# Optimization experiments

Measured on AMD Instinct MI355X. Metric: run time of the kernel, lower is better.

## Reference

```python
import jax, jax.numpy as jnp
import numpy as np

N_NODES = 20000
N_EDGES = 320000
N_FEAT = 128
HID = 64
HEADS = 4
N_CLS = 16
NEG_SLOPE = 0.2


def setup_inputs() -> dict:
    key = jax.random.key(0)
    ks = jax.random.split(key, 12)
    x = jax.random.normal(ks[0], (N_NODES, N_FEAT), dtype=jnp.float32)
    edge_index = jax.random.randint(ks[1], (2, N_EDGES), 0, N_NODES, dtype=jnp.int64)
    # layer 1: GATConv(128 -> 64, heads=4, concat)
    s1 = 1.0 / np.sqrt(N_FEAT)
    W1 = jax.random.uniform(ks[2], (N_FEAT, HEADS * HID), jnp.float32, -s1, s1)
    a_src1 = jax.random.uniform(ks[3], (HEADS, HID), jnp.float32, -s1, s1)
    a_dst1 = jax.random.uniform(ks[4], (HEADS, HID), jnp.float32, -s1, s1)
    b1 = jnp.zeros((HEADS * HID,), jnp.float32)
    # layer 2: GATConv(256 -> 16, heads=1)
    s2 = 1.0 / np.sqrt(HEADS * HID)
    W2 = jax.random.uniform(ks[5], (HEADS * HID, N_CLS), jnp.float32, -s2, s2)
    a_src2 = jax.random.uniform(ks[6], (1, N_CLS), jnp.float32, -s2, s2)
    a_dst2 = jax.random.uniform(ks[7], (1, N_CLS), jnp.float32, -s2, s2)
    b2 = jnp.zeros((N_CLS,), jnp.float32)
    return {"x": x, "edge_index": edge_index, "W1": W1, "a_src1": a_src1,
            "a_dst1": a_dst1, "b1": b1, "W2": W2, "a_src2": a_src2,
            "a_dst2": a_dst2, "b2": b2}


def gat_conv(x, src, dst, W, a_src, a_dst, bias, n_nodes):
    # x: [N, F_in]; W: [F_in, H*C]; a_src/a_dst: [H, C]
    H, C = a_src.shape
    h = (x @ W).reshape(n_nodes, H, C)                     # [N, H, C]
    al_src = jnp.sum(h * a_src[None], axis=-1)             # [N, H]
    al_dst = jnp.sum(h * a_dst[None], axis=-1)             # [N, H]
    e = jax.nn.leaky_relu(al_src[src] + al_dst[dst], NEG_SLOPE)  # [E, H]
    # segment softmax over incoming edges of each destination node
    m = jax.ops.segment_max(e, dst, num_segments=n_nodes)  # [N, H]
    e = jnp.exp(e - m[dst])
    denom = jax.ops.segment_sum(e, dst, num_segments=n_nodes)
    alpha = e / (denom[dst] + 1e-16)                       # [E, H]
    msg = h[src] * alpha[:, :, None]                       # [E, H, C]
    out = jax.ops.segment_sum(msg, dst, num_segments=n_nodes)  # [N, H, C]
    return out.reshape(n_nodes, H * C) + bias


def reference(x, edge_index, W1, a_src1, a_dst1, b1, W2, a_src2, a_dst2, b2):
    n = x.shape[0]
    loops = jnp.arange(n, dtype=edge_index.dtype)
    src = jnp.concatenate([edge_index[0], loops])
    dst = jnp.concatenate([edge_index[1], loops])
    # eval mode: dropout is identity
    h = jax.nn.elu(gat_conv(x, src, dst, W1, a_src1, a_dst1, b1, n))
    out = gat_conv(h, src, dst, W2, a_src2, a_dst2, b2, n)
    return out
```

## Files before the change

### kernel.cpp

```cpp
#include <hip/hip_runtime.h>
#include <hip/hip_bf16.h>
#include <hip/hip_fp16.h>
#include <math.h>

#define N_NODES 20000
#define N_EDGES 320000
#define E_TOT   (N_EDGES + N_NODES)
#define N_FEAT  128
#define NEG_SLOPE 0.2f
#define MAXDEG  64
#define CURPAD  16

typedef _Float16 half8 __attribute__((ext_vector_type(8)));
typedef float f32x4 __attribute__((ext_vector_type(4)));

__global__ void k_init(int* __restrict__ cur,
                       const float* __restrict__ W1, _Float16* __restrict__ W1t){
  int tid = blockIdx.x * blockDim.x + threadIdx.x;
  if (tid < N_NODES * CURPAD) cur[tid] = 0;
  if (tid < 4096){
    int n = tid >> 4, ks = tid & 15;
    union { __half2 h2[4]; half8 h8; } u;
    float v[8];
    #pragma unroll
    for (int r = 0; r < 8; ++r) v[r] = W1[(size_t)(ks * 8 + r) * 256 + n];
    u.h2[0] = __floats2half2_rn(v[0], v[1]);
    u.h2[1] = __floats2half2_rn(v[2], v[3]);
    u.h2[2] = __floats2half2_rn(v[4], v[5]);
    u.h2[3] = __floats2half2_rn(v[6], v[7]);
    *(half8*)&W1t[(size_t)n * 128 + ks * 8] = u.h8;
  }
}

__global__ __launch_bounds__(256) void k_gemm1(
                        const float* __restrict__ x, const _Float16* __restrict__ W1t,
                        const float* __restrict__ as1, const float* __restrict__ ad1,
                        _Float16* __restrict__ h1h,
                        float* __restrict__ alS, float* __restrict__ alD,
                        const int* __restrict__ ei, int* __restrict__ cur,
                        int* __restrict__ adjS){
  __shared__ _Float16 xt[64][136];
  __shared__ _Float16 Wt[128][136];
  int t  = threadIdx.x;

  {
    int fb = blockIdx.y * 313 + blockIdx.x;
    int gtid = fb * 256 + t;
    const int GSZ = 313 * 2 * 256;
    int e0 = gtid, e1 = gtid + GSZ, e2 = gtid + 2 * GSZ;
    bool k2 = (e2 < E_TOT);
    int s0, d0, s1, d1, s2 = 0, d2 = 0;
    if (e0 < N_EDGES){ s0 = ei[e0]; d0 = ei[N_EDGES + e0]; } else { s0 = d0 = e0 - N_EDGES; }
    if (e1 < N_EDGES){ s1 = ei[e1]; d1 = ei[N_EDGES + e1]; } else { s1 = d1 = e1 - N_EDGES; }
    if (k2){
      if (e2 < N_EDGES){ s2 = ei[e2]; d2 = ei[N_EDGES + e2]; } else { s2 = d2 = e2 - N_EDGES; }
    }
    int p0 = atomicAdd(&cur[d0 * CURPAD], 1);
    int p1 = atomicAdd(&cur[d1 * CURPAD], 1);
    int p2 = k2 ? atomicAdd(&cur[d2 * CURPAD], 1) : 0;
    if (p0 < MAXDEG) adjS[d0 * MAXDEG + p0] = s0;
    if (p1 < MAXDEG) adjS[d1 * MAXDEG + p1] = s1;
    if (k2 && p2 < MAXDEG) adjS[d2 * MAXDEG + p2] = s2;
  }

  int m0 = blockIdx.x * 64;
  int by = blockIdx.y;
  int j0 = by * 128;
  #pragma unroll
  for (int ii = 0; ii < 4; ++ii){
    int f = t + ii * 256;
    int r = f >> 4, s = f & 15;
    half8 xv = (half8)(_Float16)0.f;
    if (m0 + r < N_NODES){
      float4 a = *(const float4*)&x[(size_t)(m0 + r) * 128 + s * 8];
      float4 bq = *(const float4*)&x[(size_t)(m0 + r) * 128 + s * 8 + 4];
      union { __half2 h2[4]; half8 h8; } u;
      u.h2[0] = __floats2half2_rn(a.x, a.y);
      u.h2[1] = __floats2half2_rn(a.z, a.w);
      u.h2[2] = __floats2half2_rn(bq.x, bq.y);
      u.h2[3] = __floats2half2_rn(bq.z, bq.w);
      xv = u.h8;
    }
    *(half8*)&xt[r][s * 8] = xv;
  }
  #pragma unroll
  for (int ii = 0; ii < 8; ++ii){
    int f = t + ii * 256;
    int r = f >> 4, s = f & 15;
    half8 wv = *(const half8*)&W1t[(size_t)(j0 + r) * 128 + s * 8];
    *(half8*)&Wt[r][s * 8] = wv;
  }
  __syncthreads();

  int w = t >> 6, lane = t & 63;
  int g = lane >> 4, mi = lane & 15;
  f32x4 acc[8] = {};
  #pragma unroll
  for (int kk = 0; kk < 4; ++kk){
    int ko = kk * 32 + g * 8;
    half8 b = *(const half8*)&xt[w * 16 + mi][ko];
    #pragma unroll
    for (int s = 0; s < 8; ++s){
      half8 a = *(const half8*)&Wt[s * 16 + mi][ko];
      acc[s] = __builtin_amdgcn_mfma_f32_16x16x32_f16(a, b, acc[s], 0, 0, 0);
    }
  }

  int m = m0 + w * 16 + mi;
  float sA = 0.f, dA = 0.f, sB = 0.f, dB = 0.f;
  #pragma unroll
  for (int s = 0; s < 8; ++s){
    int nb = j0 + s * 16 + g * 4;
    float4 asv = *(const float4*)&as1[nb];
    float4 adv = *(const float4*)&ad1[nb];
    float sv = acc[s][0] * asv.x + acc[s][1] * asv.y + acc[s][2] * asv.z + acc[s][3] * asv.w;
    float dv = acc[s][0] * adv.x + acc[s][1] * adv.y + acc[s][2] * adv.z + acc[s][3] * adv.w;
    if (s < 4){ sA += sv; dA += dv; } else { sB += sv; dB += dv; }
    if (m < N_NODES){
      union { __half2 h2[2]; float2 f2; } u;
      u.h2[0] = __floats2half2_rn(acc[s][0], acc[s][1]);
      u.h2[1] = __floats2half2_rn(acc[s][2], acc[s][3]);
      *(float2*)&h1h[(size_t)m * 256 + nb] = u.f2;
    }
  }
  sA += __shfl_xor(sA, 16); sA += __shfl_xor(sA, 32);
  dA += __shfl_xor(dA, 16); dA += __shfl_xor(dA, 32);
  sB += __shfl_xor(sB, 16); sB += __shfl_xor(sB, 32);
  dB += __shfl_xor(dB, 16); dB += __shfl_xor(dB, 32);
  if (g == 0 && m < N_NODES){
    int h0 = by * 2, h1 = by * 2 + 1;
    alS[(size_t)h0 * N_NODES + m] = sA; alD[(size_t)h0 * N_NODES + m] = dA;
    alS[(size_t)h1 * N_NODES + m] = sB; alD[(size_t)h1 * N_NODES + m] = dB;
  }
}

__global__ __launch_bounds__(256) void k_attn1(
                        const int* __restrict__ cur, const int* __restrict__ adjS,
                        const __half* __restrict__ h1h,
                        const float* __restrict__ alS, const float* __restrict__ alD,
                        const float* __restrict__ b1, _Float16* __restrict__ heluh){
  int b    = blockIdx.x;
  int slot = b & 7;
  int h    = slot & 3;
  int g    = (slot >> 2) * 625 + (b >> 3);
  int t    = threadIdx.x;
  int w    = t >> 6, lane = t & 63;
  int grp  = lane >> 4, l16 = lane & 15;
  int hf   = l16 >> 3, l8 = l16 & 7;
  int n    = g * 16 + w * 4 + grp;

  int cnt  = cur[n * CURPAD]; cnt = (cnt > MAXDEG) ? MAXDEG : cnt;
  int base = n * MAXDEG;
  const float* __restrict__ alSp = alS + (size_t)h * N_NODES;
  float ald = alD[(size_t)h * N_NODES + n];
  const __half* __restrict__ hb = h1h + h * 64 + l8 * 8;

  float4 Aa = make_float4(0.f,0.f,0.f,0.f), Ab = Aa;
  float den = 0.f;

  int nq = cnt >> 2;
  for (int q = hf; q < nq; q += 2){
    int4 quad = *(const int4*)&adjS[base + q * 4];
    int s0 = quad.x, s1 = quad.y, s2 = quad.z, s3 = quad.w;
    float t0 = alSp[s0] + ald;
    float t1 = alSp[s1] + ald;
    float t2 = alSp[s2] + ald;
    float t3 = alSp[s3] + ald;
    t0 = (t0 > 0.f) ? t0 : NEG_SLOPE * t0;
    t1 = (t1 > 0.f) ? t1 : NEG_SLOPE * t1;
    t2 = (t2 > 0.f) ? t2 : NEG_SLOPE * t2;
    t3 = (t3 > 0.f) ? t3 : NEG_SLOPE * t3;
    float w0 = __expf(t0), w1 = __expf(t1), w2 = __expf(t2), w3 = __expf(t3);
    float4 r0 = *(const float4*)&hb[(size_t)s0 * 256];
    float4 r1 = *(const float4*)&hb[(size_t)s1 * 256];
    float4 r2 = *(const float4*)&hb[(size_t)s2 * 256];
    float4 r3 = *(const float4*)&hb[(size_t)s3 * 256];
    const __half2* p0 = (const __half2*)&r0;
    const __half2* p1 = (const __half2*)&r1;
    const __half2* p2 = (const __half2*)&r2;
    const __half2* p3 = (const __half2*)&r3;
    {
      float2 a0 = __half22float2(p0[0]), a1 = __half22float2(p0[1]);
      float2 a2 = __half22float2(p0[2]), a3 = __half22float2(p0[3]);
      Aa.x += w0 * a0.x; Aa.y += w0 * a0.y; Aa.z += w0 * a1.x; Aa.w += w0 * a1.y;
      Ab.x += w0 * a2.x; Ab.y += w0 * a2.y; Ab.z += w0 * a3.x; Ab.w += w0 * a3.y;
    }
    {
      float2 a0 = __half22float2(p1[0]), a1 = __half22float2(p1[1]);
      float2 a2 = __half22float2(p1[2]), a3 = __half22float2(p1[3]);
      Aa.x += w1 * a0.x; Aa.y += w1 * a0.y; Aa.z += w1 * a1.x; Aa.w += w1 * a1.y;
      Ab.x += w1 * a2.x; Ab.y += w1 * a2.y; Ab.z += w1 * a3.x; Ab.w += w1 * a3.y;
    }
    {
      float2 a0 = __half22float2(p2[0]), a1 = __half22float2(p2[1]);
      float2 a2 = __half22float2(p2[2]), a3 = __half22float2(p2[3]);
      Aa.x += w2 * a0.x; Aa.y += w2 * a0.y; Aa.z += w2 * a1.x; Aa.w += w2 * a1.y;
      Ab.x += w2 * a2.x; Ab.y += w2 * a2.y; Ab.z += w2 * a3.x; Ab.w += w2 * a3.y;
    }
    {
      float2 a0 = __half22float2(p3[0]), a1 = __half22float2(p3[1]);
      float2 a2 = __half22float2(p3[2]), a3 = __half22float2(p3[3]);
      Aa.x += w3 * a0.x; Aa.y += w3 * a0.y; Aa.z += w3 * a1.x; Aa.w += w3 * a1.y;
      Ab.x += w3 * a2.x; Ab.y += w3 * a2.y; Ab.z += w3 * a3.x; Ab.w += w3 * a3.y;
    }
    den += ((w0 + w1) + (w2 + w3));
  }
  if ((nq & 1) == hf){
    for (int i = base + nq * 4; i < base + cnt; ++i){
      int s0 = adjS[i];
      float t0 = alSp[s0] + ald;
      t0 = (t0 > 0.f) ? t0 : NEG_SLOPE * t0;
      float w0 = __expf(t0);
      float4 r0 = *(const float4*)&hb[(size_t)s0 * 256];
      const __half2* p0 = (const __half2*)&r0;
      float2 a0 = __half22float2(p0[0]), a1 = __half22float2(p0[1]);
      float2 a2 = __half22float2(p0[2]), a3 = __half22float2(p0[3]);
      Aa.x += w0 * a0.x; Aa.y += w0 * a0.y; Aa.z += w0 * a1.x; Aa.w += w0 * a1.y;
      Ab.x += w0 * a2.x; Ab.y += w0 * a2.y; Ab.z += w0 * a3.x; Ab.w += w0 * a3.y;
      den += w0;
    }
  }
  Aa.x += __shfl_xor(Aa.x, 8); Aa.y += __shfl_xor(Aa.y, 8);
  Aa.z += __shfl_xor(Aa.z, 8); Aa.w += __shfl_xor(Aa.w, 8);
  Ab.x += __shfl_xor(Ab.x, 8); Ab.y += __shfl_xor(Ab.y, 8);
  Ab.z += __shfl_xor(Ab.z, 8); Ab.w += __shfl_xor(Ab.w, 8);
  den  += __shfl_xor(den, 8);

  if (hf == 0){
    float rinv = 1.f / (den + 1e-16f);
    float4 bv0 = *(const float4*)&b1[h * 64 + l8 * 8];
    float4 bv1 = *(const float4*)&b1[h * 64 + l8 * 8 + 4];
    float o0 = Aa.x * rinv + bv0.x;
    float o1 = Aa.y * rinv + bv0.y;
    float o2 = Aa.z * rinv + bv0.z;
    float o3 = Aa.w * rinv + bv0.w;
    float o4 = Ab.x * rinv + bv1.x;
    float o5 = Ab.y * rinv + bv1.y;
    float o6 = Ab.z * rinv + bv1.z;
    float o7 = Ab.w * rinv + bv1.w;
    o0 = (o0 > 0.f) ? o0 : (__expf(o0) - 1.f);
    o1 = (o1 > 0.f) ? o1 : (__expf(o1) - 1.f);
    o2 = (o2 > 0.f) ? o2 : (__expf(o2) - 1.f);
    o3 = (o3 > 0.f) ? o3 : (__expf(o3) - 1.f);
    o4 = (o4 > 0.f) ? o4 : (__expf(o4) - 1.f);
    o5 = (o5 > 0.f) ? o5 : (__expf(o5) - 1.f);
    o6 = (o6 > 0.f) ? o6 : (__expf(o6) - 1.f);
    o7 = (o7 > 0.f) ? o7 : (__expf(o7) - 1.f);
    union { __half2 h2[4]; half8 h8; } u;
    u.h2[0] = __floats2half2_rn(o0, o1);
    u.h2[1] = __floats2half2_rn(o2, o3);
    u.h2[2] = __floats2half2_rn(o4, o5);
    u.h2[3] = __floats2half2_rn(o6, o7);
    *(half8*)&heluh[(size_t)n * 256 + h * 64 + l8 * 8] = u.h8;
  }
}

__global__ __launch_bounds__(256) void k_gemm2(
                        const _Float16* __restrict__ heluh, const float* __restrict__ W2,
                        const float* __restrict__ as2, const float* __restrict__ ad2,
                        float* __restrict__ h2, float* __restrict__ alS, float* __restrict__ alD){
  __shared__ _Float16 Ht[64][264];
  __shared__ _Float16 Wt[16][264];
  int t = threadIdx.x;
  int n0 = blockIdx.x * 64;
  #pragma unroll
  for (int ii = 0; ii < 8; ++ii){
    int f = t + ii * 256;
    int r = f >> 5, s = f & 31;
    half8 v = (half8)(_Float16)0.f;
    if (n0 + r < N_NODES) v = *(const half8*)&heluh[(size_t)(n0 + r) * 256 + s * 8];
    *(half8*)&Ht[r][s * 8] = v;
  }
  {
    int k = t;
    float4 w0 = *(const float4*)&W2[k * 16 + 0];
    float4 w1 = *(const float4*)&W2[k * 16 + 4];
    float4 w2 = *(const float4*)&W2[k * 16 + 8];
    float4 w3 = *(const float4*)&W2[k * 16 + 12];
    float wv[16] = {w0.x,w0.y,w0.z,w0.w, w1.x,w1.y,w1.z,w1.w,
                    w2.x,w2.y,w2.z,w2.w, w3.x,w3.y,w3.z,w3.w};
    #pragma unroll
    for (int c = 0; c < 16; ++c) Wt[c][k] = (_Float16)wv[c];
  }
  __syncthreads();

  int w = t >> 6, lane = t & 63;
  int g = lane >> 4, mi = lane & 15;
  f32x4 acc = {};
  #pragma unroll
  for (int kk = 0; kk < 8; ++kk){
    int ko = kk * 32 + g * 8;
    half8 b = *(const half8*)&Ht[w * 16 + mi][ko];
    half8 a = *(const half8*)&Wt[mi][ko];
    acc = __builtin_amdgcn_mfma_f32_16x16x32_f16(a, b, acc, 0, 0, 0);
  }
  int n = n0 + w * 16 + mi;
  float4 asv = *(const float4*)&as2[g * 4];
  float4 adv = *(const float4*)&ad2[g * 4];
  float s_ = acc[0] * asv.x + acc[1] * asv.y + acc[2] * asv.z + acc[3] * asv.w;
  float d_ = acc[0] * adv.x + acc[1] * adv.y + acc[2] * adv.z + acc[3] * adv.w;
  s_ += __shfl_xor(s_, 16); s_ += __shfl_xor(s_, 32);
  d_ += __shfl_xor(d_, 16); d_ += __shfl_xor(d_, 32);
  if (n < N_NODES){
    float4 hv = make_float4(acc[0], acc[1], acc[2], acc[3]);
    *(float4*)&h2[(size_t)n * 16 + g * 4] = hv;
    if (g == 0){ alS[n] = s_; alD[n] = d_; }
  }
}

__global__ __launch_bounds__(256) void k_attn2(
                        const int* __restrict__ cur, const int* __restrict__ adjS,
                        const float* __restrict__ h2,
                        const float* __restrict__ alS, const float* __restrict__ alD,
                        const float* __restrict__ b2, float* __restrict__ out){
  int t    = threadIdx.x;
  int w    = t >> 6, lane = t & 63;
  int grp  = lane >> 4, l16 = lane & 15;
  int j    = l16 >> 2, c4 = l16 & 3;
  int n    = blockIdx.x * 16 + w * 4 + grp;

  int cnt  = cur[n * CURPAD]; cnt = (cnt > MAXDEG) ? MAXDEG : cnt;
  int start = n * MAXDEG, end = start + cnt;
  float ald = alD[n];
  float4 acc = make_float4(0.f,0.f,0.f,0.f);
  float den = 0.f;
  for (int i = start + j; i < end; i += 4){
    int s = adjS[i];
    float tt = alS[s] + ald;
    tt = (tt > 0.f) ? tt : NEG_SLOPE * tt;
    float wv = __expf(tt);
    float4 v = *(const float4*)&h2[(size_t)s * 16 + c4 * 4];
    acc.x += wv * v.x; acc.y += wv * v.y; acc.z += wv * v.z; acc.w += wv * v.w;
    den += wv;
  }
  #pragma unroll
  for (int off = 4; off <= 8; off <<= 1){
    acc.x += __shfl_xor(acc.x, off);
    acc.y += __shfl_xor(acc.y, off);
    acc.z += __shfl_xor(acc.z, off);
    acc.w += __shfl_xor(acc.w, off);
    den   += __shfl_xor(den, off);
  }
  if (j == 0){
    float rinv = 1.f / (den + 1e-16f);
    float4 bv = *(const float4*)&b2[c4 * 4];
    float4 o;
    o.x = acc.x * rinv + bv.x; o.y = acc.y * rinv + bv.y;
    o.z = acc.z * rinv + bv.z; o.w = acc.w * rinv + bv.w;
    *(float4*)&out[(size_t)n * 16 + c4 * 4] = o;
  }
}

extern "C" void kernel_launch(void* const* d_in, const int* in_sizes, int n_in,
                              void* d_out, int out_size, void* d_ws, size_t ws_size,
                              hipStream_t stream){
  const float* x   = (const float*)d_in[0];
  const int*   ei  = (const int*)d_in[1];
  const float* W1  = (const float*)d_in[2];
  const float* as1 = (const float*)d_in[3];
  const float* ad1 = (const float*)d_in[4];
  const float* b1  = (const float*)d_in[5];
  const float* W2  = (const float*)d_in[6];
  const float* as2 = (const float*)d_in[7];
  const float* ad2 = (const float*)d_in[8];
  const float* b2  = (const float*)d_in[9];
  float* out = (float*)d_out;

  float* fws = (float*)d_ws;
  size_t off = 0;
  __half* h1h = (__half*)(fws + off); off += (size_t)N_NODES * 128;
  _Float16* W1t = (_Float16*)(fws + off); off += 256 * 64;
  _Float16* heluh = (_Float16*)(fws + off); off += (size_t)N_NODES * 128;
  float* h2   = fws + off; off += (size_t)N_NODES * 16;
  float* alS1 = fws + off; off += N_NODES * 4;
  float* alD1 = fws + off; off += N_NODES * 4;
  float* alS2 = fws + off; off += N_NODES;
  float* alD2 = fws + off; off += N_NODES;
  int* cur  = (int*)(fws + off); off += (size_t)N_NODES * CURPAD;
  int* adjS = (int*)(fws + off); off += (size_t)N_NODES * MAXDEG;

  k_init<<<(N_NODES * CURPAD + 255) / 256, 256, 0, stream>>>(cur, W1, W1t);
  k_gemm1<<<dim3(313, 2), 256, 0, stream>>>(x, W1t, as1, ad1, (_Float16*)h1h,
                                            alS1, alD1, ei, cur, adjS);
  k_attn1<<<5000, 256, 0, stream>>>(cur, adjS, h1h, alS1, alD1, b1, heluh);
  k_gemm2<<<313, 256, 0, stream>>>(heluh, W2, as2, ad2, h2, alS2, alD2);
  k_attn2<<<1250, 256, 0, stream>>>(cur, adjS, h2, alS2, alD2, b2, out);
}
```

Before: 73.25 us.

## Partition adjacency build per XCD with workgroup-scope atomics

Measured after the change: 89.61 us. 1.22x slower.

```diff
diff --git a/kernel.cpp b/kernel.cpp
--- a/kernel.cpp
+++ b/kernel.cpp
@@ -8,16 +8,15 @@
 #define E_TOT   (N_EDGES + N_NODES)
 #define N_FEAT  128
 #define NEG_SLOPE 0.2f
-#define MAXDEG  64
-#define CURPAD  16
+#define SEG     64
 
 typedef _Float16 half8 __attribute__((ext_vector_type(8)));
 typedef float f32x4 __attribute__((ext_vector_type(4)));
 
-__global__ void k_init(int* __restrict__ cur,
+__global__ void k_init(int* __restrict__ cur8,
                        const float* __restrict__ W1, _Float16* __restrict__ W1t){
   int tid = blockIdx.x * blockDim.x + threadIdx.x;
-  if (tid < N_NODES * CURPAD) cur[tid] = 0;
+  if (tid < 8 * N_NODES) cur8[tid] = 0;
   if (tid < 4096){
     int n = tid >> 4, ks = tid & 15;
     union { __half2 h2[4]; half8 h8; } u;
@@ -37,13 +36,18 @@
                         const float* __restrict__ as1, const float* __restrict__ ad1,
                         _Float16* __restrict__ h1h,
                         float* __restrict__ alS, float* __restrict__ alD,
-                        const int* __restrict__ ei, int* __restrict__ cur,
-                        int* __restrict__ adjS){
+                        const int* __restrict__ ei, int* __restrict__ cur8,
+                        int* __restrict__ adjS8){
   __shared__ _Float16 xt[64][136];
   __shared__ _Float16 Wt[128][136];
   int t  = threadIdx.x;
 
   {
+    int xcd;
+    asm volatile("s_getreg_b32 %0, hwreg(HW_REG_XCC_ID)" : "=s"(xcd));
+    xcd &= 7;
+    int* __restrict__ curp = cur8 + xcd * N_NODES;
+    int* __restrict__ adjp = adjS8 + (size_t)xcd * N_NODES * SEG;
     int fb = blockIdx.y * 313 + blockIdx.x;
     int gtid = fb * 256 + t;
     const int GSZ = 313 * 2 * 256;
@@ -55,12 +59,12 @@
     if (k2){
       if (e2 < N_EDGES){ s2 = ei[e2]; d2 = ei[N_EDGES + e2]; } else { s2 = d2 = e2 - N_EDGES; }
     }
-    int p0 = atomicAdd(&cur[d0 * CURPAD], 1);
-    int p1 = atomicAdd(&cur[d1 * CURPAD], 1);
-    int p2 = k2 ? atomicAdd(&cur[d2 * CURPAD], 1) : 0;
-    if (p0 < MAXDEG) adjS[d0 * MAXDEG + p0] = s0;
-    if (p1 < MAXDEG) adjS[d1 * MAXDEG + p1] = s1;
-    if (k2 && p2 < MAXDEG) adjS[d2 * MAXDEG + p2] = s2;
+    int p0 = __hip_atomic_fetch_add(&curp[d0], 1, __ATOMIC_RELAXED, __HIP_MEMORY_SCOPE_WORKGROUP);
+    int p1 = __hip_atomic_fetch_add(&curp[d1], 1, __ATOMIC_RELAXED, __HIP_MEMORY_SCOPE_WORKGROUP);
+    int p2 = k2 ? __hip_atomic_fetch_add(&curp[d2], 1, __ATOMIC_RELAXED, __HIP_MEMORY_SCOPE_WORKGROUP) : 0;
+    if (p0 < SEG) adjp[(size_t)d0 * SEG + p0] = s0;
+    if (p1 < SEG) adjp[(size_t)d1 * SEG + p1] = s1;
+    if (k2 && p2 < SEG) adjp[(size_t)d2 * SEG + p2] = s2;
   }
 
   int m0 = blockIdx.x * 64;
@@ -135,7 +139,7 @@
 }
 
 __global__ __launch_bounds__(256) void k_attn1(
-                        const int* __restrict__ cur, const int* __restrict__ adjS,
+                        const int* __restrict__ cur8, const int* __restrict__ adjS8,
                         const __half* __restrict__ h1h,
                         const float* __restrict__ alS, const float* __restrict__ alD,
                         const float* __restrict__ b1, _Float16* __restrict__ heluh){
@@ -149,8 +153,6 @@
   int hf   = l16 >> 3, l8 = l16 & 7;
   int n    = g * 16 + w * 4 + grp;
 
-  int cnt  = cur[n * CURPAD]; cnt = (cnt > MAXDEG) ? MAXDEG : cnt;
-  int base = n * MAXDEG;
   const float* __restrict__ alSp = alS + (size_t)h * N_NODES;
   float ald = alD[(size_t)h * N_NODES + n];
   const __half* __restrict__ hb = h1h + h * 64 + l8 * 8;
@@ -158,56 +160,37 @@
   float4 Aa = make_float4(0.f,0.f,0.f,0.f), Ab = Aa;
   float den = 0.f;
 
-  int nq = cnt >> 2;
-  for (int q = hf; q < nq; q += 2){
-    int4 quad = *(const int4*)&adjS[base + q * 4];
-    int s0 = quad.x, s1 = quad.y, s2 = quad.z, s3 = quad.w;
-    float t0 = alSp[s0] + ald;
-    float t1 = alSp[s1] + ald;
-    float t2 = alSp[s2] + ald;
-    float t3 = alSp[s3] + ald;
-    t0 = (t0 > 0.f) ? t0 : NEG_SLOPE * t0;
-    t1 = (t1 > 0.f) ? t1 : NEG_SLOPE * t1;
-    t2 = (t2 > 0.f) ? t2 : NEG_SLOPE * t2;
-    t3 = (t3 > 0.f) ? t3 : NEG_SLOPE * t3;
-    float w0 = __expf(t0), w1 = __expf(t1), w2 = __expf(t2), w3 = __expf(t3);
-    float4 r0 = *(const float4*)&hb[(size_t)s0 * 256];
-    float4 r1 = *(const float4*)&hb[(size_t)s1 * 256];
-    float4 r2 = *(const float4*)&hb[(size_t)s2 * 256];
-    float4 r3 = *(const float4*)&hb[(size_t)s3 * 256];
-    const __half2* p0 = (const __half2*)&r0;
-    const __half2* p1 = (const __half2*)&r1;
-    const __half2* p2 = (const __half2*)&r2;
-    const __half2* p3 = (const __half2*)&r3;
-    {
-      float2 a0 = __half22float2(p0[0]), a1 = __half22float2(p0[1]);
-      float2 a2 = __half22float2(p0[2]), a3 = __half22float2(p0[3]);
-      Aa.x += w0 * a0.x; Aa.y += w0 * a0.y; Aa.z += w0 * a1.x; Aa.w += w0 * a1.y;
-      Ab.x += w0 * a2.x; Ab.y += w0 * a2.y; Ab.z += w0 * a3.x; Ab.w += w0 * a3.y;
-    }
-    {
-      float2 a0 = __half22float2(p1[0]), a1 = __half22float2(p1[1]);
-      float2 a2 = __half22float2(p1[2]), a3 = __half22float2(p1[3]);
-      Aa.x += w1 * a0.x; Aa.y += w1 * a0.y; Aa.z += w1 * a1.x; Aa.w += w1 * a1.y;
-      Ab.x += w1 * a2.x; Ab.y += w1 * a2.y; Ab.z += w1 * a3.x; Ab.w += w1 * a3.y;
-    }
-    {
-      float2 a0 = __half22float2(p2[0]), a1 = __half22float2(p2[1]);
-      float2 a2 = __half22float2(p2[2]), a3 = __half22float2(p2[3]);
-      Aa.x += w2 * a0.x; Aa.y += w2 * a0.y; Aa.z += w2 * a1.x; Aa.w += w2 * a1.y;
-      Ab.x += w2 * a2.x; Ab.y += w2 * a2.y; Ab.z += w2 * a3.x; Ab.w += w2 * a3.y;
-    }
-    {
-      float2 a0 = __half22float2(p3[0]), a1 = __half22float2(p3[1]);
-      float2 a2 = __half22float2(p3[2]), a3 = __half22float2(p3[3]);
-      Aa.x += w3 * a0.x; Aa.y += w3 * a0.y; Aa.z += w3 * a1.x; Aa.w += w3 * a1.y;
-      Ab.x += w3 * a2.x; Ab.y += w3 * a2.y; Ab.z += w3 * a3.x; Ab.w += w3 * a3.y;
-    }
-    den += ((w0 + w1) + (w2 + w3));
-  }
-  if ((nq & 1) == hf){
-    for (int i = base + nq * 4; i < base + cnt; ++i){
-      int s0 = adjS[i];
+  for (int xs = hf; xs < 8; xs += 2){
+    int cnt = cur8[xs * N_NODES + n]; cnt = (cnt > SEG) ? SEG : cnt;
+    const int* __restrict__ ap = adjS8 + ((size_t)xs * N_NODES + n) * SEG;
+    int i = 0;
+    for (; i + 1 < cnt; i += 2){
+      int s0 = ap[i], s1 = ap[i + 1];
+      float t0 = alSp[s0] + ald;
+      float t1 = alSp[s1] + ald;
+      t0 = (t0 > 0.f) ? t0 : NEG_SLOPE * t0;
+      t1 = (t1 > 0.f) ? t1 : NEG_SLOPE * t1;
+      float w0 = __expf(t0), w1 = __expf(t1);
+      float4 r0 = *(const float4*)&hb[(size_t)s0 * 256];
+      float4 r1 = *(const float4*)&hb[(size_t)s1 * 256];
+      const __half2* p0 = (const __half2*)&r0;
+      const __half2* p1 = (const __half2*)&r1;
+      {
+        float2 a0 = __half22float2(p0[0]), a1 = __half22float2(p0[1]);
+        float2 a2 = __half22float2(p0[2]), a3 = __half22float2(p0[3]);
+        Aa.x += w0 * a0.x; Aa.y += w0 * a0.y; Aa.z += w0 * a1.x; Aa.w += w0 * a1.y;
+        Ab.x += w0 * a2.x; Ab.y += w0 * a2.y; Ab.z += w0 * a3.x; Ab.w += w0 * a3.y;
+      }
+      {
+        float2 a0 = __half22float2(p1[0]), a1 = __half22float2(p1[1]);
+        float2 a2 = __half22float2(p1[2]), a3 = __half22float2(p1[3]);
+        Aa.x += w1 * a0.x; Aa.y += w1 * a0.y; Aa.z += w1 * a1.x; Aa.w += w1 * a1.y;
+        Ab.x += w1 * a2.x; Ab.y += w1 * a2.y; Ab.z += w1 * a3.x; Ab.w += w1 * a3.y;
+      }
+      den += (w0 + w1);
+    }
+    if (i < cnt){
+      int s0 = ap[i];
       float t0 = alSp[s0] + ald;
       t0 = (t0 > 0.f) ? t0 : NEG_SLOPE * t0;
       float w0 = __expf(t0);
@@ -309,7 +292,7 @@
 }
 
 __global__ __launch_bounds__(256) void k_attn2(
-                        const int* __restrict__ cur, const int* __restrict__ adjS,
+                        const int* __restrict__ cur8, const int* __restrict__ adjS8,
                         const float* __restrict__ h2,
                         const float* __restrict__ alS, const float* __restrict__ alD,
                         const float* __restrict__ b2, float* __restrict__ out){
@@ -319,19 +302,21 @@
   int j    = l16 >> 2, c4 = l16 & 3;
   int n    = blockIdx.x * 16 + w * 4 + grp;
 
-  int cnt  = cur[n * CURPAD]; cnt = (cnt > MAXDEG) ? MAXDEG : cnt;
-  int start = n * MAXDEG, end = start + cnt;
   float ald = alD[n];
   float4 acc = make_float4(0.f,0.f,0.f,0.f);
   float den = 0.f;
-  for (int i = start + j; i < end; i += 4){
-    int s = adjS[i];
-    float tt = alS[s] + ald;
-    tt = (tt > 0.f) ? tt : NEG_SLOPE * tt;
-    float wv = __expf(tt);
-    float4 v = *(const float4*)&h2[(size_t)s * 16 + c4 * 4];
-    acc.x += wv * v.x; acc.y += wv * v.y; acc.z += wv * v.z; acc.w += wv * v.w;
-    den += wv;
+  for (int xs = j; xs < 8; xs += 4){
+    int cnt = cur8[xs * N_NODES + n]; cnt = (cnt > SEG) ? SEG : cnt;
+    const int* __restrict__ ap = adjS8 + ((size_t)xs * N_NODES + n) * SEG;
+    for (int i = 0; i < cnt; ++i){
+      int s = ap[i];
+      float tt = alS[s] + ald;
+      tt = (tt > 0.f) ? tt : NEG_SLOPE * tt;
+      float wv = __expf(tt);
+      float4 v = *(const float4*)&h2[(size_t)s * 16 + c4 * 4];
+      acc.x += wv * v.x; acc.y += wv * v.y; acc.z += wv * v.z; acc.w += wv * v.w;
+      den += wv;
+    }
   }
   #pragma unroll
   for (int off = 4; off <= 8; off <<= 1){
@@ -376,13 +361,13 @@
   float* alD1 = fws + off; off += N_NODES * 4;
   float* alS2 = fws + off; off += N_NODES;
   float* alD2 = fws + off; off += N_NODES;
-  int* cur  = (int*)(fws + off); off += (size_t)N_NODES * CURPAD;
-  int* adjS = (int*)(fws + off); off += (size_t)N_NODES * MAXDEG;
-
-  k_init<<<(N_NODES * CURPAD + 255) / 256, 256, 0, stream>>>(cur, W1, W1t);
+  int* cur8  = (int*)(fws + off); off += (size_t)8 * N_NODES;
+  int* adjS8 = (int*)(fws + off); off += (size_t)8 * N_NODES * SEG;
+
+  k_init<<<(8 * N_NODES + 255) / 256, 256, 0, stream>>>(cur8, W1, W1t);
   k_gemm1<<<dim3(313, 2), 256, 0, stream>>>(x, W1t, as1, ad1, (_Float16*)h1h,
-                                            alS1, alD1, ei, cur, adjS);
-  k_attn1<<<5000, 256, 0, stream>>>(cur, adjS, h1h, alS1, alD1, b1, heluh);
+                                            alS1, alD1, ei, cur8, adjS8);
+  k_attn1<<<5000, 256, 0, stream>>>(cur8, adjS8, h1h, alS1, alD1, b1, heluh);
   k_gemm2<<<313, 256, 0, stream>>>(heluh, W2, as2, ad2, h2, alS2, alD2);
-  k_attn2<<<1250, 256, 0, stream>>>(cur, adjS, h2, alS2, alD2, b2, out);
-}
+  k_attn2<<<1250, 256, 0, stream>>>(cur8, adjS8, h2, alS2, alD2, b2, out);
+}
```
